# Kernel tuning notes

Measured on AMD Instinct MI355X. Metric: run time of the kernel, lower is better.

Reference implementation:

```python
import jax, jax.numpy as jnp
import numpy as np

S, B, D, H, DH, E, F = 2048, 2, 512, 8, 64, 8, 1024
TOPK = 2


def setup_inputs() -> dict:
    key = jax.random.key(0)
    ks = jax.random.split(key, 12)
    rn = lambda k, shp, s=0.02: jax.random.normal(k, shp, jnp.float32) * s
    # RoPE tables (half-split convention): (S, DH)
    pos = jnp.arange(S, dtype=jnp.float32)[:, None]
    inv_freq = 1.0 / (10000.0 ** (jnp.arange(0, DH, 2, dtype=jnp.float32) / DH))
    ang = pos * inv_freq[None, :]                       # (S, DH//2)
    cos = jnp.concatenate([jnp.cos(ang), jnp.cos(ang)], axis=-1)
    sin = jnp.concatenate([jnp.sin(ang), jnp.sin(ang)], axis=-1)
    return {
        "src": jax.random.normal(ks[0], (S, B, D), jnp.float32),
        "cos": cos, "sin": sin,
        "Wq": rn(ks[1], (D, D)), "bq": jnp.zeros((D,), jnp.float32),
        "Wk": rn(ks[2], (D, D)), "bk": jnp.zeros((D,), jnp.float32),
        "Wv": rn(ks[3], (D, D)), "bv": jnp.zeros((D,), jnp.float32),
        "Wo": rn(ks[4], (D, D)), "bo": jnp.zeros((D,), jnp.float32),
        "ln1_g": jnp.ones((D,), jnp.float32), "ln1_b": jnp.zeros((D,), jnp.float32),
        "ln2_g": jnp.ones((D,), jnp.float32), "ln2_b": jnp.zeros((D,), jnp.float32),
        "Wg": rn(ks[5], (D, E)),
        "W1": rn(ks[6], (E, D, F)), "B1": jnp.zeros((E, F), jnp.float32),
        "W2": rn(ks[7], (E, F, D)), "B2": jnp.zeros((E, D), jnp.float32),
    }


def _layernorm(x, g, b, eps=1e-5):
    m = x.mean(-1, keepdims=True)
    v = ((x - m) ** 2).mean(-1, keepdims=True)
    return (x - m) * jax.lax.rsqrt(v + eps) * g + b


def _rotate_half(x):
    x1, x2 = jnp.split(x, 2, axis=-1)
    return jnp.concatenate([-x2, x1], axis=-1)


def _forward(src, cos, sin, Wq, bq, Wk, bk, Wv, bv, Wo, bo,
             ln1_g, ln1_b, ln2_g, ln2_b, Wg, W1, B1, W2, B2):
    # ---- RoPE self-attention ----
    q = (src @ Wq + bq).reshape(S, B, H, DH)
    k = (src @ Wk + bk).reshape(S, B, H, DH)
    v = (src @ Wv + bv).reshape(S, B, H, DH)
    c = cos[:, None, None, :]
    s = sin[:, None, None, :]
    q = q * c + _rotate_half(q) * s
    k = k * c + _rotate_half(k) * s
    scores = jnp.einsum("sbhd,tbhd->bhst", q, k) / jnp.sqrt(jnp.float32(DH))
    attn = jax.nn.softmax(scores, axis=-1)              # (B,H,S,S)
    ctx = jnp.einsum("bhst,tbhd->sbhd", attn, v).reshape(S, B, D)
    attn_out = ctx @ Wo + bo
    x = _layernorm(src + attn_out, ln1_g, ln1_b)
    # ---- MoE feed-forward (top-k softmax gating) ----
    xt = x.reshape(S * B, D)                            # (N, D)
    probs = jax.nn.softmax(xt @ Wg, axis=-1)            # (N, E)
    top_v, top_i = jax.lax.top_k(probs, TOPK)           # (N, TOPK)
    top_v = top_v / top_v.sum(-1, keepdims=True)
    N = S * B
    gates = jnp.zeros((N, E), jnp.float32).at[
        jnp.arange(N)[:, None], top_i].add(top_v)       # (N, E)
    h = jax.nn.relu(jnp.einsum("nd,edf->nef", xt, W1) + B1[None])   # (N,E,F)
    eo = jnp.einsum("nef,efd->ned", h, W2) + B2[None]               # (N,E,D)
    moe_out = jnp.einsum("ne,ned->nd", gates, eo).reshape(S, B, D)
    return _layernorm(x + moe_out, ln2_g, ln2_b)


def reference(src, cos, sin, Wq, bq, Wk, bk, Wv, bv, Wo, bo,
              ln1_g, ln1_b, ln2_g, ln2_b, Wg, W1, B1, W2, B2):
    return _forward(src, cos, sin, Wq, bq, Wk, bk, Wv, bv, Wo, bo,
                    ln1_g, ln1_b, ln2_g, ln2_b, Wg, W1, B1, W2, B2)
```

## Files before the change

kernel.cpp:

```cpp
#include <hip/hip_runtime.h>
#include <math.h>

#define S_  2048
#define B_  2
#define D_  512
#define H_  8
#define DH_ 64
#define E_  8
#define F_  1024
#define N_  4096
#define NPAIR_ 8192

typedef __attribute__((ext_vector_type(4))) float f32x4;
typedef __attribute__((ext_vector_type(8))) short short8;
typedef unsigned short u16;

__device__ __forceinline__ u16 f2bf(float f) {
  unsigned u = __builtin_bit_cast(unsigned, f);
  u += 0x7fffu + ((u >> 16) & 1u);
  return (u16)(u >> 16);
}
__device__ __forceinline__ float bf2f(u16 h) {
  unsigned u = ((unsigned)h) << 16;
  return __builtin_bit_cast(float, u);
}

__global__ __launch_bounds__(256) void src_split(const float* __restrict__ in,
                                                 u16* __restrict__ hi,
                                                 u16* __restrict__ lo) {
  size_t i = ((size_t)blockIdx.x * 256 + threadIdx.x) * 8;
  float f[8];
  *(float4*)&f[0] = *(const float4*)&in[i];
  *(float4*)&f[4] = *(const float4*)&in[i + 4];
  short8 h, l;
#pragma unroll
  for (int j = 0; j < 8; ++j) {
    u16 a = f2bf(f[j]);
    h[j] = (short)a;
    l[j] = (short)f2bf(f[j] - bf2f(a));
  }
  *(short8*)&hi[i] = h;
  *(short8*)&lo[i] = l;
}

__global__ __launch_bounds__(256) void wsplit_t(const float* __restrict__ W,
                                                u16* __restrict__ Whi,
                                                u16* __restrict__ Wlo,
                                                int Nn, int K) {
  __shared__ u16 Th[64][72];
  __shared__ u16 Tl[64][72];
  int kb = blockIdx.y * 64, nb = blockIdx.x * 64;
  int r = threadIdx.x >> 2, c0 = (threadIdx.x & 3) * 16;
  const float* wp = &W[(size_t)(kb + r) * Nn + nb + c0];
#pragma unroll
  for (int c = 0; c < 16; c += 4) {
    float4 t = *(const float4*)&wp[c];
    float f[4] = {t.x, t.y, t.z, t.w};
#pragma unroll
    for (int j = 0; j < 4; ++j) {
      u16 a = f2bf(f[j]);
      Th[r][c0 + c + j] = a;
      Tl[r][c0 + c + j] = f2bf(f[j] - bf2f(a));
    }
  }
  __syncthreads();
  short8 h0, h1, l0, l1;
#pragma unroll
  for (int j = 0; j < 8; ++j) {
    h0[j] = (short)Th[c0 + j][r];     h1[j] = (short)Th[c0 + 8 + j][r];
    l0[j] = (short)Tl[c0 + j][r];     l1[j] = (short)Tl[c0 + 8 + j][r];
  }
  size_t ob = (size_t)(nb + r) * K + kb + c0;
  *(short8*)&Whi[ob] = h0;  *(short8*)&Whi[ob + 8] = h1;
  *(short8*)&Wlo[ob] = l0;  *(short8*)&Wlo[ob + 8] = l1;
}

__global__ __launch_bounds__(256) void wtrans(const float* __restrict__ W,
                                              u16* __restrict__ Wt,
                                              int K, int Nn) {
  size_t eo = (size_t)blockIdx.z * K * Nn;
  __shared__ u16 T[64][72];
  int kb = blockIdx.y * 64, nb = blockIdx.x * 64;
  int r = threadIdx.x >> 2, c0 = (threadIdx.x & 3) * 16;
  const float* wp = &W[eo + (size_t)(kb + r) * Nn + nb + c0];
#pragma unroll
  for (int c = 0; c < 16; c += 4) {
    float4 t = *(const float4*)&wp[c];
    T[r][c0 + c + 0] = f2bf(t.x);
    T[r][c0 + c + 1] = f2bf(t.y);
    T[r][c0 + c + 2] = f2bf(t.z);
    T[r][c0 + c + 3] = f2bf(t.w);
  }
  __syncthreads();
  short8 s0, s1;
#pragma unroll
  for (int j = 0; j < 8; ++j) {
    s0[j] = (short)T[c0 + j][r];
    s1[j] = (short)T[c0 + 8 + j][r];
  }
  *(short8*)&Wt[eo + (size_t)(nb + r) * K + kb + c0] = s0;
  *(short8*)&Wt[eo + (size_t)(nb + r) * K + kb + c0 + 8] = s1;
}

__global__ __launch_bounds__(256) void qkv_mfma(const u16* __restrict__ Ah_g,
                                                const u16* __restrict__ Al_g,
                                                const u16* __restrict__ Bh_g,
                                                const u16* __restrict__ Bl_g,
                                                const float* __restrict__ bq,
                                                const float* __restrict__ bk,
                                                const float* __restrict__ bv,
                                                const float* __restrict__ cosb,
                                                const float* __restrict__ sinb,
                                                u16* __restrict__ qh, u16* __restrict__ ql,
                                                u16* __restrict__ kh, u16* __restrict__ kl,
                                                u16* __restrict__ vb) {
  __shared__ u16 Ah[128][40], Al[128][40], Bh[128][40], Bl[128][40];
  int tid = threadIdx.x;
  int w = tid >> 6, l = tid & 63;
  int wr = w >> 1, wc = w & 1;
  int lg = l >> 4, lx = l & 15;
  int m0 = blockIdx.x * 128, n0 = blockIdx.y * 128;
  int sr = tid >> 1, s16 = (tid & 1) * 16;
  const u16* Aph = Ah_g + (size_t)(m0 + sr) * 512;
  const u16* Apl = Al_g + (size_t)(m0 + sr) * 512;
  const u16* Bph = Bh_g + (size_t)(n0 + sr) * 512;
  const u16* Bpl = Bl_g + (size_t)(n0 + sr) * 512;
  f32x4 acc[4][4];
#pragma unroll
  for (int m = 0; m < 4; ++m)
#pragma unroll
    for (int n = 0; n < 4; ++n) acc[m][n] = (f32x4){0.f, 0.f, 0.f, 0.f};
  short8 ah0 = *(const short8*)&Aph[s16];
  short8 ah1 = *(const short8*)&Aph[s16 + 8];
  short8 al0 = *(const short8*)&Apl[s16];
  short8 al1 = *(const short8*)&Apl[s16 + 8];
  short8 bh0 = *(const short8*)&Bph[s16];
  short8 bh1 = *(const short8*)&Bph[s16 + 8];
  short8 bl0 = *(const short8*)&Bpl[s16];
  short8 bl1 = *(const short8*)&Bpl[s16 + 8];
  for (int k0 = 0; k0 < 512; k0 += 32) {
    __syncthreads();
    *(short8*)&Ah[sr][s16] = ah0; *(short8*)&Ah[sr][s16 + 8] = ah1;
    *(short8*)&Al[sr][s16] = al0; *(short8*)&Al[sr][s16 + 8] = al1;
    *(short8*)&Bh[sr][s16] = bh0; *(short8*)&Bh[sr][s16 + 8] = bh1;
    *(short8*)&Bl[sr][s16] = bl0; *(short8*)&Bl[sr][s16 + 8] = bl1;
    __syncthreads();
    if (k0 + 32 < 512) {
      int ko = k0 + 32 + s16;
      ah0 = *(const short8*)&Aph[ko]; ah1 = *(const short8*)&Aph[ko + 8];
      al0 = *(const short8*)&Apl[ko]; al1 = *(const short8*)&Apl[ko + 8];
      bh0 = *(const short8*)&Bph[ko]; bh1 = *(const short8*)&Bph[ko + 8];
      bl0 = *(const short8*)&Bpl[ko]; bl1 = *(const short8*)&Bpl[ko + 8];
    }
    short8 fah[4], fal[4], fbh[4], fbl[4];
#pragma unroll
    for (int m = 0; m < 4; ++m) {
      fah[m] = *(const short8*)&Ah[wr * 64 + m * 16 + lx][lg * 8];
      fal[m] = *(const short8*)&Al[wr * 64 + m * 16 + lx][lg * 8];
    }
#pragma unroll
    for (int n = 0; n < 4; ++n) {
      fbh[n] = *(const short8*)&Bh[wc * 64 + n * 16 + lx][lg * 8];
      fbl[n] = *(const short8*)&Bl[wc * 64 + n * 16 + lx][lg * 8];
    }
#pragma unroll
    for (int m = 0; m < 4; ++m)
#pragma unroll
      for (int n = 0; n < 4; ++n) {
        acc[m][n] = __builtin_amdgcn_mfma_f32_16x16x32_bf16(fah[m], fbh[n], acc[m][n], 0, 0, 0);
        acc[m][n] = __builtin_amdgcn_mfma_f32_16x16x32_bf16(fal[m], fbh[n], acc[m][n], 0, 0, 0);
        acc[m][n] = __builtin_amdgcn_mfma_f32_16x16x32_bf16(fah[m], fbl[n], acc[m][n], 0, 0, 0);
      }
  }
  int tcolbase = n0 + wc * 64;
  int tsel = tcolbase >> 9;
  int hbase = tcolbase & 511;
  const float* bias = (tsel == 0) ? bq : (tsel == 1) ? bk : bv;
  if (tsel == 2) {
#pragma unroll
    for (int m = 0; m < 4; ++m)
#pragma unroll
      for (int i = 0; i < 4; ++i) {
        int row = m0 + wr * 64 + m * 16 + lg * 4 + i;
#pragma unroll
        for (int n = 0; n < 4; ++n) {
          int col = hbase + n * 16 + lx;
          vb[(size_t)row * 512 + col] = f2bf(acc[m][n][i] + bias[col]);
        }
      }
  } else {
    u16* oh = tsel ? kh : qh;
    u16* ol = tsel ? kl : ql;
    float qsc = tsel ? 1.f : 0.125f;
#pragma unroll
    for (int m = 0; m < 4; ++m)
#pragma unroll
      for (int i = 0; i < 4; ++i) {
        int row = m0 + wr * 64 + m * 16 + lg * 4 + i;
        int s = row >> 1;
#pragma unroll
        for (int n = 0; n < 2; ++n) {
          int dln = n * 16 + lx;
          float c  = cosb[s * 64 + dln];
          float sn = sinb[s * 64 + dln];
          float a  = acc[m][n][i]     + bias[hbase + dln];
          float b2 = acc[m][n + 2][i] + bias[hbase + dln + 32];
          float ra = (a * c - b2 * sn) * qsc;
          float rb = (b2 * c + a * sn) * qsc;
          size_t ix = (size_t)row * 512 + hbase + dln;
          u16 rah = f2bf(ra);
          oh[ix] = rah; ol[ix] = f2bf(ra - bf2f(rah));
          u16 rbh = f2bf(rb);
          oh[ix + 32] = rbh; ol[ix + 32] = f2bf(rb - bf2f(rbh));
        }
      }
  }
}

__global__ __launch_bounds__(512) void attn_mfma2(const u16* __restrict__ qh,
                                                  const u16* __restrict__ ql,
                                                  const u16* __restrict__ kh,
                                                  const u16* __restrict__ kl,
                                                  const u16* __restrict__ vbuf,
                                                  u16* __restrict__ poh,
                                                  u16* __restrict__ pol,
                                                  float* __restrict__ pml) {
  __shared__ u16 Khi[64][72];
  __shared__ u16 Klo[64][72];
  __shared__ u16 Vt[64][72];
  __shared__ unsigned P2[8][16][32];
  int tid = threadIdx.x;
  int w = tid >> 6, l = tid & 63;
  int lg = l >> 4, lx = l & 15;
  int f = blockIdx.x;
  int xcd = f & 7, j = f >> 3;
  int slab = xcd + 8 * (j & 3);
  int qt = j >> 2;
  int bh = slab >> 1, kvh = slab & 1;
  int b = bh >> 3, h = bh & 7;

  short8 qfh[2], qfl[2];
  {
    int qrow = qt * 128 + w * 16 + lx;
    size_t qo = (size_t)(qrow * 2 + b) * 512 + h * 64 + lg * 8;
    qfh[0] = *(const short8*)&qh[qo];
    qfh[1] = *(const short8*)&qh[qo + 32];
    qfl[0] = *(const short8*)&ql[qo];
    qfl[1] = *(const short8*)&ql[qo + 32];
  }

  f32x4 o_acc[4];
#pragma unroll
  for (int dg = 0; dg < 4; ++dg) o_acc[dg] = (f32x4){0.f, 0.f, 0.f, 0.f};
  float m_run = -1e30f, l_run = 0.f;

  int kvr = tid >> 3, ds4 = (tid & 7) * 8;
  int kvc = tid & 63, dsg = (tid >> 6) * 8;
  int psw = (lx & 7) << 2;

  short8 rkh, rkl, rv;
  {
    int t0 = kvh * 1024;
    size_t ko = (size_t)((t0 + kvr) * 2 + b) * 512 + h * 64 + ds4;
    rkh = *(const short8*)&kh[ko];
    rkl = *(const short8*)&kl[ko];
    size_t vo = (size_t)((t0 + kvc) * 2 + b) * 512 + h * 64 + dsg;
    rv = *(const short8*)&vbuf[vo];
  }

  for (int tt = 0; tt < 1024; tt += 64) {
    __syncthreads();
    *(short8*)&Khi[kvr][ds4] = rkh;
    *(short8*)&Klo[kvr][ds4] = rkl;
#pragma unroll
    for (int c = 0; c < 8; ++c) Vt[dsg + c][kvc] = (u16)rv[c];
    __syncthreads();
    if (tt + 64 < 1024) {
      int t0 = kvh * 1024 + tt + 64;
      size_t ko = (size_t)((t0 + kvr) * 2 + b) * 512 + h * 64 + ds4;
      rkh = *(const short8*)&kh[ko];
      rkl = *(const short8*)&kl[ko];
      size_t vo = (size_t)((t0 + kvc) * 2 + b) * 512 + h * 64 + dsg;
      rv = *(const short8*)&vbuf[vo];
    }

    f32x4 sc[4];
#pragma unroll
    for (int cg = 0; cg < 4; ++cg) {
      short8 kf0 = *(const short8*)&Khi[cg * 16 + lx][lg * 8];
      short8 kf1 = *(const short8*)&Khi[cg * 16 + lx][32 + lg * 8];
      short8 kg0 = *(const short8*)&Klo[cg * 16 + lx][lg * 8];
      short8 kg1 = *(const short8*)&Klo[cg * 16 + lx][32 + lg * 8];
      f32x4 a = (f32x4){0.f, 0.f, 0.f, 0.f};
      a = __builtin_amdgcn_mfma_f32_16x16x32_bf16(kf0, qfh[0], a, 0, 0, 0);
      a = __builtin_amdgcn_mfma_f32_16x16x32_bf16(kf1, qfh[1], a, 0, 0, 0);
      a = __builtin_amdgcn_mfma_f32_16x16x32_bf16(kf0, qfl[0], a, 0, 0, 0);
      a = __builtin_amdgcn_mfma_f32_16x16x32_bf16(kf1, qfl[1], a, 0, 0, 0);
      a = __builtin_amdgcn_mfma_f32_16x16x32_bf16(kg0, qfh[0], a, 0, 0, 0);
      a = __builtin_amdgcn_mfma_f32_16x16x32_bf16(kg1, qfh[1], a, 0, 0, 0);
      sc[cg] = a;
    }

    float tm = sc[0][0];
#pragma unroll
    for (int cg = 0; cg < 4; ++cg)
#pragma unroll
      for (int i = 0; i < 4; ++i) tm = fmaxf(tm, sc[cg][i]);
    tm = fmaxf(tm, __shfl_xor(tm, 16));
    tm = fmaxf(tm, __shfl_xor(tm, 32));
    float mn = fmaxf(m_run, tm);
    float corr = __expf(m_run - mn);
    m_run = mn;
    float ts = 0.f;
#pragma unroll
    for (int cg = 0; cg < 4; ++cg)
#pragma unroll
      for (int i = 0; i < 4; ++i) {
        float pv = __expf(sc[cg][i] - mn);
        sc[cg][i] = pv;
        ts += pv;
      }
    ts += __shfl_xor(ts, 16);
    ts += __shfl_xor(ts, 32);
    l_run = l_run * corr + ts;
#pragma unroll
    for (int dg = 0; dg < 4; ++dg) o_acc[dg] *= corr;

#pragma unroll
    for (int cg = 0; cg < 4; ++cg)
#pragma unroll
      for (int t = 0; t < 2; ++t) {
        unsigned dw = (unsigned)f2bf(sc[cg][2 * t]) |
                      ((unsigned)f2bf(sc[cg][2 * t + 1]) << 16);
        P2[w][lx][(8 * cg + 2 * lg + t) ^ psw] = dw;
      }
    short8 pf0 = *(const short8*)&P2[w][lx][(4 * lg) ^ psw];
    short8 pf1 = *(const short8*)&P2[w][lx][(16 + 4 * lg) ^ psw];

#pragma unroll
    for (int dg = 0; dg < 4; ++dg) {
      short8 v0 = *(const short8*)&Vt[dg * 16 + lx][lg * 8];
      short8 v1 = *(const short8*)&Vt[dg * 16 + lx][32 + lg * 8];
      o_acc[dg] = __builtin_amdgcn_mfma_f32_16x16x32_bf16(v0, pf0, o_acc[dg], 0, 0, 0);
      o_acc[dg] = __builtin_amdgcn_mfma_f32_16x16x32_bf16(v1, pf1, o_acc[dg], 0, 0, 0);
    }
  }

  {
    int qrow = qt * 128 + w * 16 + lx;
    int row2 = qrow * 2 + b;
    size_t base = (size_t)kvh * ((size_t)N_ * D_) + (size_t)row2 * 512 + h * 64;
#pragma unroll
    for (int dg = 0; dg < 4; ++dg)
#pragma unroll
      for (int i = 0; i < 4; ++i) {
        int d = dg * 16 + 4 * lg + i;
        float val = o_acc[dg][i];
        u16 hi = f2bf(val);
        poh[base + d] = hi;
        pol[base + d] = f2bf(val - bf2f(hi));
      }
    if (lg == 0) {
      int u = row2 * 8 + h;
      pml[(size_t)kvh * 65536 + u * 2 + 0] = m_run;
      pml[(size_t)kvh * 65536 + u * 2 + 1] = l_run;
    }
  }
}

__global__ __launch_bounds__(256) void merge_attn2(const u16* __restrict__ poh,
                                                   const u16* __restrict__ pol,
                                                   const float* __restrict__ pml,
                                                   u16* __restrict__ ch,
                                                   u16* __restrict__ cl) {
  int u = blockIdx.x * 4 + (threadIdx.x >> 6);
  int lane = threadIdx.x & 63;
  float m0 = pml[u * 2], l0 = pml[u * 2 + 1];
  float m1 = pml[65536 + u * 2], l1 = pml[65536 + u * 2 + 1];
  float m = fmaxf(m0, m1);
  float e0 = __expf(m0 - m), e1 = __expf(m1 - m);
  float inv = 1.f / (l0 * e0 + l1 * e1);
  int n = u >> 3, h = u & 7;
  size_t base = (size_t)n * 512 + h * 64 + lane;
  const size_t PO1 = (size_t)N_ * D_;
  float v0 = bf2f(poh[base]) + bf2f(pol[base]);
  float v1 = bf2f(poh[PO1 + base]) + bf2f(pol[PO1 + base]);
  float val = (v0 * e0 + v1 * e1) * inv;
  u16 hi = f2bf(val);
  ch[base] = hi;
  cl[base] = f2bf(val - bf2f(hi));
}

__global__ __launch_bounds__(256) void wo_mfma(const u16* __restrict__ Ah_g,
                                               const u16* __restrict__ Al_g,
                                               const u16* __restrict__ Bh_g,
                                               const u16* __restrict__ Bl_g,
                                               const float* __restrict__ bias,
                                               float* __restrict__ C) {
  __shared__ u16 Ah[128][40], Al[128][40], Bh[128][40], Bl[128][40];
  int tid = threadIdx.x;
  int w = tid >> 6, l = tid & 63;
  int wr = w >> 1, wc = w & 1;
  int lg = l >> 4, lx = l & 15;
  int m0 = blockIdx.x * 128, n0 = blockIdx.y * 128;
  int sr = tid >> 1, s16 = (tid & 1) * 16;
  const u16* Aph = Ah_g + (size_t)(m0 + sr) * 512;
  const u16* Apl = Al_g + (size_t)(m0 + sr) * 512;
  const u16* Bph = Bh_g + (size_t)(n0 + sr) * 512;
  const u16* Bpl = Bl_g + (size_t)(n0 + sr) * 512;
  f32x4 acc[4][4];
#pragma unroll
  for (int m = 0; m < 4; ++m)
#pragma unroll
    for (int n = 0; n < 4; ++n) acc[m][n] = (f32x4){0.f, 0.f, 0.f, 0.f};
  short8 ah0 = *(const short8*)&Aph[s16];
  short8 ah1 = *(const short8*)&Aph[s16 + 8];
  short8 al0 = *(const short8*)&Apl[s16];
  short8 al1 = *(const short8*)&Apl[s16 + 8];
  short8 bh0 = *(const short8*)&Bph[s16];
  short8 bh1 = *(const short8*)&Bph[s16 + 8];
  short8 bl0 = *(const short8*)&Bpl[s16];
  short8 bl1 = *(const short8*)&Bpl[s16 + 8];
  for (int k0 = 0; k0 < 512; k0 += 32) {
    __syncthreads();
    *(short8*)&Ah[sr][s16] = ah0; *(short8*)&Ah[sr][s16 + 8] = ah1;
    *(short8*)&Al[sr][s16] = al0; *(short8*)&Al[sr][s16 + 8] = al1;
    *(short8*)&Bh[sr][s16] = bh0; *(short8*)&Bh[sr][s16 + 8] = bh1;
    *(short8*)&Bl[sr][s16] = bl0; *(short8*)&Bl[sr][s16 + 8] = bl1;
    __syncthreads();
    if (k0 + 32 < 512) {
      int ko = k0 + 32 + s16;
      ah0 = *(const short8*)&Aph[ko]; ah1 = *(const short8*)&Aph[ko + 8];
      al0 = *(const short8*)&Apl[ko]; al1 = *(const short8*)&Apl[ko + 8];
      bh0 = *(const short8*)&Bph[ko]; bh1 = *(const short8*)&Bph[ko + 8];
      bl0 = *(const short8*)&Bpl[ko]; bl1 = *(const short8*)&Bpl[ko + 8];
    }
    short8 fah[4], fal[4], fbh[4], fbl[4];
#pragma unroll
    for (int m = 0; m < 4; ++m) {
      fah[m] = *(const short8*)&Ah[wr * 64 + m * 16 + lx][lg * 8];
      fal[m] = *(const short8*)&Al[wr * 64 + m * 16 + lx][lg * 8];
    }
#pragma unroll
    for (int n = 0; n < 4; ++n) {
      fbh[n] = *(const short8*)&Bh[wc * 64 + n * 16 + lx][lg * 8];
      fbl[n] = *(const short8*)&Bl[wc * 64 + n * 16 + lx][lg * 8];
    }
#pragma unroll
    for (int m = 0; m < 4; ++m)
#pragma unroll
      for (int n = 0; n < 4; ++n) {
        acc[m][n] = __builtin_amdgcn_mfma_f32_16x16x32_bf16(fah[m], fbh[n], acc[m][n], 0, 0, 0);
        acc[m][n] = __builtin_amdgcn_mfma_f32_16x16x32_bf16(fal[m], fbh[n], acc[m][n], 0, 0, 0);
        acc[m][n] = __builtin_amdgcn_mfma_f32_16x16x32_bf16(fah[m], fbl[n], acc[m][n], 0, 0, 0);
      }
  }
#pragma unroll
  for (int m = 0; m < 4; ++m)
#pragma unroll
    for (int i = 0; i < 4; ++i) {
      int row = m0 + wr * 64 + m * 16 + lg * 4 + i;
#pragma unroll
      for (int n = 0; n < 4; ++n) {
        int col = n0 + wc * 64 + n * 16 + lx;
        C[(size_t)row * 512 + col] = acc[m][n][i] + bias[col];
      }
    }
}

__global__ __launch_bounds__(256) void ln_res_gate(const float* __restrict__ a,
                                                   const float* __restrict__ b,
                                                   const float* __restrict__ g,
                                                   const float* __restrict__ beta,
                                                   const float* __restrict__ Wg,
                                                   float* __restrict__ out,
                                                   u16* __restrict__ obf,
                                                   float* __restrict__ gp,
                                                   int* __restrict__ tope) {
  int n = blockIdx.x * 4 + (threadIdx.x >> 6);
  int lane = threadIdx.x & 63;
  float v[8];
  float s = 0.f;
#pragma unroll
  for (int i = 0; i < 8; ++i) {
    int d = lane + 64 * i;
    v[i] = a[(size_t)n * D_ + d] + b[(size_t)n * D_ + d];
    s += v[i];
  }
#pragma unroll
  for (int m = 32; m; m >>= 1) s += __shfl_xor(s, m);
  float mean = s * (1.f / D_);
  float s2 = 0.f;
#pragma unroll
  for (int i = 0; i < 8; ++i) { float t = v[i] - mean; s2 += t * t; }
#pragma unroll
  for (int m = 32; m; m >>= 1) s2 += __shfl_xor(s2, m);
  float r = rsqrtf(s2 * (1.f / D_) + 1e-5f);
  float p[E_] = {};
#pragma unroll
  for (int i = 0; i < 8; ++i) {
    int d = lane + 64 * i;
    float val = (v[i] - mean) * r * g[d] + beta[d];
    out[(size_t)n * D_ + d] = val;
    obf[(size_t)n * D_ + d] = f2bf(val);
    const float* wr = &Wg[(size_t)d * E_];
#pragma unroll
    for (int e = 0; e < E_; ++e) p[e] += val * wr[e];
  }
#pragma unroll
  for (int e = 0; e < E_; ++e)
#pragma unroll
    for (int m = 32; m; m >>= 1) p[e] += __shfl_xor(p[e], m);
  if (lane == 0) {
    float mx = p[0];
#pragma unroll
    for (int e = 1; e < E_; ++e) mx = fmaxf(mx, p[e]);
    float q[E_];
#pragma unroll
    for (int e = 0; e < E_; ++e) q[e] = expf(p[e] - mx);
    int e1 = 0;
#pragma unroll
    for (int e = 1; e < E_; ++e) if (q[e] > q[e1]) e1 = e;
    int e2 = (e1 == 0) ? 1 : 0;
#pragma unroll
    for (int e = 0; e < E_; ++e) if (e != e1 && q[e] > q[e2]) e2 = e;
    float denom = q[e1] + q[e2];
    gp[n * 2] = q[e1] / denom;
    gp[n * 2 + 1] = q[e2] / denom;
    tope[n] = e1 | (e2 << 8);
  }
}

__global__ __launch_bounds__(256) void ln2_final(const float* __restrict__ x,
                                                 const u16* __restrict__ mp,
                                                 const float* __restrict__ g,
                                                 const float* __restrict__ beta,
                                                 float* __restrict__ out) {
  int n = blockIdx.x * 4 + (threadIdx.x >> 6);
  int lane = threadIdx.x & 63;
  float v[8];
  float s = 0.f;
#pragma unroll
  for (int i = 0; i < 8; ++i) {
    int d = lane + 64 * i;
    v[i] = x[(size_t)n * D_ + d] + bf2f(mp[(size_t)(2 * n) * D_ + d]) +
           bf2f(mp[(size_t)(2 * n + 1) * D_ + d]);
    s += v[i];
  }
#pragma unroll
  for (int m = 32; m; m >>= 1) s += __shfl_xor(s, m);
  float mean = s * (1.f / D_);
  float s2 = 0.f;
#pragma unroll
  for (int i = 0; i < 8; ++i) { float t = v[i] - mean; s2 += t * t; }
#pragma unroll
  for (int m = 32; m; m >>= 1) s2 += __shfl_xor(s2, m);
  float r = rsqrtf(s2 * (1.f / D_) + 1e-5f);
#pragma unroll
  for (int i = 0; i < 8; ++i) {
    int d = lane + 64 * i;
    out[(size_t)n * D_ + d] = (v[i] - mean) * r * g[d] + beta[d];
  }
}

__global__ __launch_bounds__(256) void route_build(const int* __restrict__ tope,
                                                   int* __restrict__ cnt,
                                                   int* __restrict__ lst) {
  int e = blockIdx.x;
  __shared__ int wsum[4];
  __shared__ int basem;
  int tid = threadIdx.x;
  int w = tid >> 6, lane = tid & 63;
  if (tid == 0) basem = 0;
  __syncthreads();
  for (int c0 = 0; c0 < N_; c0 += 256) {
    int n = c0 + tid;
    int te = tope[n];
    int e1 = te & 0xff, e2 = (te >> 8) & 0xff;
    bool m2 = (e2 == e);
    bool flag = (e1 == e) || m2;
    unsigned long long mask = __ballot(flag);
    int wpre = __popcll(mask & ((1ull << lane) - 1ull));
    if (lane == 0) wsum[w] = __popcll(mask);
    __syncthreads();
    int woff = 0;
    for (int i = 0; i < w; ++i) woff += wsum[i];
    int total = wsum[0] + wsum[1] + wsum[2] + wsum[3];
    if (flag) lst[e * N_ + basem + woff + wpre] = n * 2 + (m2 ? 1 : 0);
    __syncthreads();
    if (tid == 0) basem += total;
    __syncthreads();
  }
  if (tid == 0) cnt[e] = basem;
}

template <int MODE>
__global__ __launch_bounds__(256) void moe_mfma(const u16* __restrict__ Abase,
                                                const u16* __restrict__ Wt,
                                                const float* __restrict__ bias,
                                                const float* __restrict__ gp,
                                                u16* __restrict__ outp,
                                                const int* __restrict__ cnt,
                                                const int* __restrict__ lst) {
  constexpr int K  = MODE ? 1024 : 512;
  constexpr int Nn = MODE ? 512 : 1024;
  constexpr int NT = Nn / 128;
  constexpr int NI = K / 32;
  int fidx = blockIdx.x;
  int e = fidx & 7;
  int r = fidx >> 3;
  int nt = r % NT;
  int mt = r / NT;
  int c = cnt[e];
  int m0 = mt * 64;
  if (m0 >= c) return;
  int off = 0;
#pragma unroll
  for (int i = 0; i < E_; ++i) if (i < e) off += cnt[i];
  int n0 = nt * 128;
  __shared__ u16 As[64][40];
  __shared__ u16 Bs[128][40];
  int tid = threadIdx.x;
  int w = tid >> 6, l = tid & 63;
  int lg = l >> 4, lx = l & 15;
  int arow = tid >> 2, aseg = (tid & 3) * 8;
  int brow = tid >> 1, bseg = (tid & 1) * 16;
  int ar = m0 + arow; if (ar >= c) ar = c - 1;
  const u16* Ap;
  if (MODE == 0) Ap = Abase + (size_t)(lst[e * N_ + ar] >> 1) * 512 + aseg;
  else           Ap = Abase + (size_t)(off + ar) * 1024 + aseg;
  const u16* Bp = Wt + (size_t)e * K * Nn + (size_t)(n0 + brow) * K + bseg;

  f32x4 acc[4][2];
#pragma unroll
  for (int m = 0; m < 4; ++m)
#pragma unroll
    for (int n = 0; n < 2; ++n) acc[m][n] = (f32x4){0.f, 0.f, 0.f, 0.f};

  short8 pa  = *(const short8*)&Ap[0];
  short8 pb0 = *(const short8*)&Bp[0];
  short8 pb1 = *(const short8*)&Bp[8];
  for (int kk = 0; kk < NI; ++kk) {
    __syncthreads();
    *(short8*)&As[arow][aseg] = pa;
    *(short8*)&Bs[brow][bseg] = pb0;
    *(short8*)&Bs[brow][bseg + 8] = pb1;
    __syncthreads();
    if (kk + 1 < NI) {
      int ko = (kk + 1) * 32;
      pa  = *(const short8*)&Ap[ko];
      pb0 = *(const short8*)&Bp[ko];
      pb1 = *(const short8*)&Bp[ko + 8];
    }
    short8 af[4], bf[2];
#pragma unroll
    for (int m = 0; m < 4; ++m)
      af[m] = *(const short8*)&As[m * 16 + lx][lg * 8];
#pragma unroll
    for (int n = 0; n < 2; ++n)
      bf[n] = *(const short8*)&Bs[w * 32 + n * 16 + lx][lg * 8];
#pragma unroll
    for (int m = 0; m < 4; ++m)
#pragma unroll
      for (int n = 0; n < 2; ++n)
        acc[m][n] = __builtin_amdgcn_mfma_f32_16x16x32_bf16(af[m], bf[n], acc[m][n], 0, 0, 0);
  }
#pragma unroll
  for (int m = 0; m < 4; ++m)
#pragma unroll
    for (int i = 0; i < 4; ++i) {
      int rr = m0 + m * 16 + lg * 4 + i;
      if (rr < c) {
#pragma unroll
        for (int n = 0; n < 2; ++n) {
          int col = n0 + w * 32 + n * 16 + lx;
          float val = acc[m][n][i] + bias[e * Nn + col];
          if (MODE == 0) {
            outp[(size_t)(off + rr) * 1024 + col] = f2bf(fmaxf(val, 0.f));
          } else {
            int p = lst[e * N_ + rr];
            outp[(size_t)p * 512 + col] = f2bf(gp[p] * val);
          }
        }
      }
    }
}

extern "C" void kernel_launch(void* const* d_in, const int* in_sizes, int n_in,
                              void* d_out, int out_size, void* d_ws, size_t ws_size,
                              hipStream_t stream) {
  const float* src  = (const float*)d_in[0];
  const float* cosb = (const float*)d_in[1];
  const float* sinb = (const float*)d_in[2];
  const float* Wq   = (const float*)d_in[3];
  const float* bq   = (const float*)d_in[4];
  const float* Wk   = (const float*)d_in[5];
  const float* bk   = (const float*)d_in[6];
  const float* Wv   = (const float*)d_in[7];
  const float* bv   = (const float*)d_in[8];
  const float* Wo   = (const float*)d_in[9];
  const float* bo   = (const float*)d_in[10];
  const float* ln1g = (const float*)d_in[11];
  const float* ln1b = (const float*)d_in[12];
  const float* ln2g = (const float*)d_in[13];
  const float* ln2b = (const float*)d_in[14];
  const float* Wg   = (const float*)d_in[15];
  const float* W1   = (const float*)d_in[16];
  const float* B1   = (const float*)d_in[17];
  const float* W2   = (const float*)d_in[18];
  const float* B2   = (const float*)d_in[19];
  float* out = (float*)d_out;
  char* wsb = (char*)d_ws;

  const size_t MB1 = 1u << 20;
  u16* sh   = (u16*)(wsb + 0 * MB1);
  u16* sl   = (u16*)(wsb + 4 * MB1);
  u16* qhb  = (u16*)(wsb + 8 * MB1);
  u16* qlb  = (u16*)(wsb + 12 * MB1);
  u16* khb  = (u16*)(wsb + 16 * MB1);
  u16* klb  = (u16*)(wsb + 20 * MB1);
  u16* vbuf = (u16*)(wsb + 24 * MB1);
  u16* poh  = (u16*)(wsb + 28 * MB1);
  u16* pol  = (u16*)(wsb + 36 * MB1);
  float* pml = (float*)(wsb + 44 * MB1);
  float* aob = (float*)(wsb + 28 * MB1);
  float* xb  = (float*)(wsb + 36 * MB1);
  u16* xbf   = (u16*)(wsb + 44 * MB1);
  u16* Wqkv_hi = (u16*)(wsb + 48 * MB1);
  u16* Wqkv_lo = (u16*)(wsb + 48 * MB1 + 1572864);
  u16* Wo_hi   = (u16*)(wsb + 48 * MB1 + 3145728);
  u16* Wo_lo   = (u16*)(wsb + 48 * MB1 + 3670016);
  u16* W1t     = (u16*)(wsb + 52 * MB1);
  u16* W2t     = (u16*)(wsb + 28 * MB1);
  float* gpb   = (float*)(wsb + 60 * MB1);
  int* cnt     = (int*)(wsb + 60 * MB1 + 32768);
  int* lst     = (int*)(wsb + 60 * MB1 + 32768 + 64);
  int* tope    = (int*)(wsb + 60 * MB1 + 32768 + 64 + 131072);
  u16* ch  = sh;
  u16* cl  = sl;
  u16* hbf = (u16*)(wsb + 8 * MB1);
  u16* mp  = (u16*)(wsb + 0 * MB1);

  dim3 blk(256);
  src_split<<<dim3(1024), blk, 0, stream>>>(src, sh, sl);
  wsplit_t<<<dim3(8, 8), blk, 0, stream>>>(Wq, Wqkv_hi, Wqkv_lo, 512, 512);
  wsplit_t<<<dim3(8, 8), blk, 0, stream>>>(Wk, Wqkv_hi + 512 * 512, Wqkv_lo + 512 * 512, 512, 512);
  wsplit_t<<<dim3(8, 8), blk, 0, stream>>>(Wv, Wqkv_hi + 1024 * 512, Wqkv_lo + 1024 * 512, 512, 512);
  wsplit_t<<<dim3(8, 8), blk, 0, stream>>>(Wo, Wo_hi, Wo_lo, 512, 512);
  qkv_mfma<<<dim3(32, 12), blk, 0, stream>>>(sh, sl, Wqkv_hi, Wqkv_lo, bq, bk, bv,
                                             cosb, sinb, qhb, qlb, khb, klb, vbuf);
  attn_mfma2<<<dim3(512), dim3(512), 0, stream>>>(qhb, qlb, khb, klb, vbuf, poh, pol, pml);
  merge_attn2<<<dim3(8192), blk, 0, stream>>>(poh, pol, pml, ch, cl);
  wo_mfma<<<dim3(32, 4), blk, 0, stream>>>(ch, cl, Wo_hi, Wo_lo, bo, aob);
  ln_res_gate<<<dim3(1024), blk, 0, stream>>>(src, aob, ln1g, ln1b, Wg, xb, xbf, gpb, tope);
  wtrans<<<dim3(8, 16, 8), blk, 0, stream>>>(W2, W2t, 1024, 512);
  wtrans<<<dim3(16, 8, 8), blk, 0, stream>>>(W1, W1t, 512, 1024);
  route_build<<<dim3(8), blk, 0, stream>>>(tope, cnt, lst);
  moe_mfma<0><<<dim3(8 * 8 * 64), blk, 0, stream>>>(xbf, W1t, B1, gpb, hbf, cnt, lst);
  moe_mfma<1><<<dim3(8 * 4 * 64), blk, 0, stream>>>(hbf, W2t, B2, gpb, mp, cnt, lst);
  ln2_final<<<dim3(1024), blk, 0, stream>>>(xb, mp, ln2g, ln2b, out);
}
```

Before: 227.2 us.

## Double-buffer attention K/V tiles and XCD-swizzle GEMM block mapping

The attention kernel now keeps two LDS buffers for K/V tiles, so the next tile is written to shared memory while the current one is consumed. This drops one of the two barriers per iteration. The QKV and Wo GEMMs switch to a 1D grid whose mapping puts four consecutive M-tiles on each XCD, aiming to improve L2 reuse of A rows. LDS use in the attention kernel roughly doubles for K/V, which may lower occupancy.

```diff
diff --git a/kernel.cpp b/kernel.cpp
--- a/kernel.cpp
+++ b/kernel.cpp
@@ -119,7 +119,11 @@
   int w = tid >> 6, l = tid & 63;
   int wr = w >> 1, wc = w & 1;
   int lg = l >> 4, lx = l & 15;
-  int m0 = blockIdx.x * 128, n0 = blockIdx.y * 128;
+  int f = blockIdx.x;
+  int xcd = f & 7, rr = f >> 3;
+  int mt = xcd * 4 + (rr & 3);
+  int nt = rr >> 2;
+  int m0 = mt * 128, n0 = nt * 128;
   int sr = tid >> 1, s16 = (tid & 1) * 16;
   const u16* Aph = Ah_g + (size_t)(m0 + sr) * 512;
   const u16* Apl = Al_g + (size_t)(m0 + sr) * 512;
@@ -225,9 +229,9 @@
                                                   u16* __restrict__ poh,
                                                   u16* __restrict__ pol,
                                                   float* __restrict__ pml) {
-  __shared__ u16 Khi[64][72];
-  __shared__ u16 Klo[64][72];
-  __shared__ u16 Vt[64][72];
+  __shared__ u16 Khi[2][64][72];
+  __shared__ u16 Klo[2][64][72];
+  __shared__ u16 Vt[2][64][72];
   __shared__ unsigned P2[8][16][32];
   int tid = threadIdx.x;
   int w = tid >> 6, l = tid & 63;
@@ -266,31 +270,43 @@
     rkl = *(const short8*)&kl[ko];
     size_t vo = (size_t)((t0 + kvc) * 2 + b) * 512 + h * 64 + dsg;
     rv = *(const short8*)&vbuf[vo];
-  }
-
-  for (int tt = 0; tt < 1024; tt += 64) {
-    __syncthreads();
-    *(short8*)&Khi[kvr][ds4] = rkh;
-    *(short8*)&Klo[kvr][ds4] = rkl;
-#pragma unroll
-    for (int c = 0; c < 8; ++c) Vt[dsg + c][kvc] = (u16)rv[c];
-    __syncthreads();
-    if (tt + 64 < 1024) {
-      int t0 = kvh * 1024 + tt + 64;
-      size_t ko = (size_t)((t0 + kvr) * 2 + b) * 512 + h * 64 + ds4;
-      rkh = *(const short8*)&kh[ko];
-      rkl = *(const short8*)&kl[ko];
-      size_t vo = (size_t)((t0 + kvc) * 2 + b) * 512 + h * 64 + dsg;
-      rv = *(const short8*)&vbuf[vo];
+    *(short8*)&Khi[0][kvr][ds4] = rkh;
+    *(short8*)&Klo[0][kvr][ds4] = rkl;
+#pragma unroll
+    for (int c = 0; c < 8; ++c) Vt[0][dsg + c][kvc] = (u16)rv[c];
+    t0 += 64;
+    ko = (size_t)((t0 + kvr) * 2 + b) * 512 + h * 64 + ds4;
+    rkh = *(const short8*)&kh[ko];
+    rkl = *(const short8*)&kl[ko];
+    vo = (size_t)((t0 + kvc) * 2 + b) * 512 + h * 64 + dsg;
+    rv = *(const short8*)&vbuf[vo];
+  }
+
+  for (int it = 0; it < 16; ++it) {
+    int cur = it & 1;
+    __syncthreads();
+    if (it + 1 < 16) {
+      *(short8*)&Khi[cur ^ 1][kvr][ds4] = rkh;
+      *(short8*)&Klo[cur ^ 1][kvr][ds4] = rkl;
+#pragma unroll
+      for (int c = 0; c < 8; ++c) Vt[cur ^ 1][dsg + c][kvc] = (u16)rv[c];
+      if (it + 2 < 16) {
+        int t0 = kvh * 1024 + (it + 2) * 64;
+        size_t ko = (size_t)((t0 + kvr) * 2 + b) * 512 + h * 64 + ds4;
+        rkh = *(const short8*)&kh[ko];
+        rkl = *(const short8*)&kl[ko];
+        size_t vo = (size_t)((t0 + kvc) * 2 + b) * 512 + h * 64 + dsg;
+        rv = *(const short8*)&vbuf[vo];
+      }
     }
 
     f32x4 sc[4];
 #pragma unroll
     for (int cg = 0; cg < 4; ++cg) {
-      short8 kf0 = *(const short8*)&Khi[cg * 16 + lx][lg * 8];
-      short8 kf1 = *(const short8*)&Khi[cg * 16 + lx][32 + lg * 8];
-      short8 kg0 = *(const short8*)&Klo[cg * 16 + lx][lg * 8];
-      short8 kg1 = *(const short8*)&Klo[cg * 16 + lx][32 + lg * 8];
+      short8 kf0 = *(const short8*)&Khi[cur][cg * 16 + lx][lg * 8];
+      short8 kf1 = *(const short8*)&Khi[cur][cg * 16 + lx][32 + lg * 8];
+      short8 kg0 = *(const short8*)&Klo[cur][cg * 16 + lx][lg * 8];
+      short8 kg1 = *(const short8*)&Klo[cur][cg * 16 + lx][32 + lg * 8];
       f32x4 a = (f32x4){0.f, 0.f, 0.f, 0.f};
       a = __builtin_amdgcn_mfma_f32_16x16x32_bf16(kf0, qfh[0], a, 0, 0, 0);
       a = __builtin_amdgcn_mfma_f32_16x16x32_bf16(kf1, qfh[1], a, 0, 0, 0);
@@ -339,8 +355,8 @@
 
 #pragma unroll
     for (int dg = 0; dg < 4; ++dg) {
-      short8 v0 = *(const short8*)&Vt[dg * 16 + lx][lg * 8];
-      short8 v1 = *(const short8*)&Vt[dg * 16 + lx][32 + lg * 8];
+      short8 v0 = *(const short8*)&Vt[cur][dg * 16 + lx][lg * 8];
+      short8 v1 = *(const short8*)&Vt[cur][dg * 16 + lx][32 + lg * 8];
       o_acc[dg] = __builtin_amdgcn_mfma_f32_16x16x32_bf16(v0, pf0, o_acc[dg], 0, 0, 0);
       o_acc[dg] = __builtin_amdgcn_mfma_f32_16x16x32_bf16(v1, pf1, o_acc[dg], 0, 0, 0);
     }
@@ -402,7 +418,10 @@
   int w = tid >> 6, l = tid & 63;
   int wr = w >> 1, wc = w & 1;
   int lg = l >> 4, lx = l & 15;
-  int m0 = blockIdx.x * 128, n0 = blockIdx.y * 128;
+  int f = blockIdx.x;
+  int xcd = f & 7, rr = f >> 3;
+  int m0 = (xcd * 4 + (rr & 3)) * 128;
+  int n0 = (rr >> 2) * 128;
   int sr = tid >> 1, s16 = (tid & 1) * 16;
   const u16* Aph = Ah_g + (size_t)(m0 + sr) * 512;
   const u16* Apl = Al_g + (size_t)(m0 + sr) * 512;
@@ -747,11 +766,11 @@
   wsplit_t<<<dim3(8, 8), blk, 0, stream>>>(Wk, Wqkv_hi + 512 * 512, Wqkv_lo + 512 * 512, 512, 512);
   wsplit_t<<<dim3(8, 8), blk, 0, stream>>>(Wv, Wqkv_hi + 1024 * 512, Wqkv_lo + 1024 * 512, 512, 512);
   wsplit_t<<<dim3(8, 8), blk, 0, stream>>>(Wo, Wo_hi, Wo_lo, 512, 512);
-  qkv_mfma<<<dim3(32, 12), blk, 0, stream>>>(sh, sl, Wqkv_hi, Wqkv_lo, bq, bk, bv,
-                                             cosb, sinb, qhb, qlb, khb, klb, vbuf);
+  qkv_mfma<<<dim3(384), blk, 0, stream>>>(sh, sl, Wqkv_hi, Wqkv_lo, bq, bk, bv,
+                                          cosb, sinb, qhb, qlb, khb, klb, vbuf);
   attn_mfma2<<<dim3(512), dim3(512), 0, stream>>>(qhb, qlb, khb, klb, vbuf, poh, pol, pml);
   merge_attn2<<<dim3(8192), blk, 0, stream>>>(poh, pol, pml, ch, cl);
-  wo_mfma<<<dim3(32, 4), blk, 0, stream>>>(ch, cl, Wo_hi, Wo_lo, bo, aob);
+  wo_mfma<<<dim3(128), blk, 0, stream>>>(ch, cl, Wo_hi, Wo_lo, bo, aob);
   ln_res_gate<<<dim3(1024), blk, 0, stream>>>(src, aob, ln1g, ln1b, Wg, xb, xbf, gpb, tope);
   wtrans<<<dim3(8, 16, 8), blk, 0, stream>>>(W2, W2t, 1024, 512);
   wtrans<<<dim3(16, 8, 8), blk, 0, stream>>>(W1, W1t, 512, 1024);
```

New measurement: 226.9 us. About the same (-0.1%).

## Split attention KV into four chunks and remap GEMM blocks per XCD

Applied to the files above, without the earlier changes.

Attention now splits the key/value sequence into four 512-token chunks instead of two, doubling the grid to 1024 blocks, and the merge kernel combines four partial results. The qkv and wo GEMMs use a 1D grid remapped so each XCD handles a contiguous group of M tiles, which should improve L2 reuse. The MFMA sections get s_setprio hints, P stores are widened to 64-bit with a new swizzle, and the workspace layout is reshuffled to hold the larger partial buffers. Trade-offs are more partial-output traffic and a heavier merge pass in exchange for better occupancy in attention.

```diff
diff --git a/kernel.cpp b/kernel.cpp
--- a/kernel.cpp
+++ b/kernel.cpp
@@ -119,7 +119,11 @@
   int w = tid >> 6, l = tid & 63;
   int wr = w >> 1, wc = w & 1;
   int lg = l >> 4, lx = l & 15;
-  int m0 = blockIdx.x * 128, n0 = blockIdx.y * 128;
+  int f = blockIdx.x;
+  int xcd = f & 7, rr = f >> 3;
+  int mt = xcd * 4 + (rr & 3);
+  int nt = rr >> 2;
+  int m0 = mt * 128, n0 = nt * 128;
   int sr = tid >> 1, s16 = (tid & 1) * 16;
   const u16* Aph = Ah_g + (size_t)(m0 + sr) * 512;
   const u16* Apl = Al_g + (size_t)(m0 + sr) * 512;
@@ -234,9 +238,9 @@
   int lg = l >> 4, lx = l & 15;
   int f = blockIdx.x;
   int xcd = f & 7, j = f >> 3;
-  int slab = xcd + 8 * (j & 3);
-  int qt = j >> 2;
-  int bh = slab >> 1, kvh = slab & 1;
+  int slab = xcd + 8 * (j & 7);
+  int qt = j >> 3;
+  int bh = slab >> 2, kvh = slab & 3;
   int b = bh >> 3, h = bh & 7;
 
   short8 qfh[2], qfl[2];
@@ -256,11 +260,11 @@
 
   int kvr = tid >> 3, ds4 = (tid & 7) * 8;
   int kvc = tid & 63, dsg = (tid >> 6) * 8;
-  int psw = (lx & 7) << 2;
+  int psw = (lx & 3) << 3;
 
   short8 rkh, rkl, rv;
   {
-    int t0 = kvh * 1024;
+    int t0 = kvh * 512;
     size_t ko = (size_t)((t0 + kvr) * 2 + b) * 512 + h * 64 + ds4;
     rkh = *(const short8*)&kh[ko];
     rkl = *(const short8*)&kl[ko];
@@ -268,15 +272,15 @@
     rv = *(const short8*)&vbuf[vo];
   }
 
-  for (int tt = 0; tt < 1024; tt += 64) {
+  for (int tt = 0; tt < 512; tt += 64) {
     __syncthreads();
     *(short8*)&Khi[kvr][ds4] = rkh;
     *(short8*)&Klo[kvr][ds4] = rkl;
 #pragma unroll
     for (int c = 0; c < 8; ++c) Vt[dsg + c][kvc] = (u16)rv[c];
     __syncthreads();
-    if (tt + 64 < 1024) {
-      int t0 = kvh * 1024 + tt + 64;
+    if (tt + 64 < 512) {
+      int t0 = kvh * 512 + tt + 64;
       size_t ko = (size_t)((t0 + kvr) * 2 + b) * 512 + h * 64 + ds4;
       rkh = *(const short8*)&kh[ko];
       rkl = *(const short8*)&kl[ko];
@@ -285,6 +289,7 @@
     }
 
     f32x4 sc[4];
+    __builtin_amdgcn_s_setprio(1);
 #pragma unroll
     for (int cg = 0; cg < 4; ++cg) {
       short8 kf0 = *(const short8*)&Khi[cg * 16 + lx][lg * 8];
@@ -300,6 +305,7 @@
       a = __builtin_amdgcn_mfma_f32_16x16x32_bf16(kg1, qfh[1], a, 0, 0, 0);
       sc[cg] = a;
     }
+    __builtin_amdgcn_s_setprio(0);
 
     float tm = sc[0][0];
 #pragma unroll
@@ -327,16 +333,16 @@
     for (int dg = 0; dg < 4; ++dg) o_acc[dg] *= corr;
 
 #pragma unroll
-    for (int cg = 0; cg < 4; ++cg)
-#pragma unroll
-      for (int t = 0; t < 2; ++t) {
-        unsigned dw = (unsigned)f2bf(sc[cg][2 * t]) |
-                      ((unsigned)f2bf(sc[cg][2 * t + 1]) << 16);
-        P2[w][lx][(8 * cg + 2 * lg + t) ^ psw] = dw;
-      }
+    for (int cg = 0; cg < 4; ++cg) {
+      unsigned d0 = (unsigned)f2bf(sc[cg][0]) | ((unsigned)f2bf(sc[cg][1]) << 16);
+      unsigned d1 = (unsigned)f2bf(sc[cg][2]) | ((unsigned)f2bf(sc[cg][3]) << 16);
+      uint2 dd; dd.x = d0; dd.y = d1;
+      *(uint2*)&P2[w][lx][(8 * cg + 2 * lg) ^ psw] = dd;
+    }
     short8 pf0 = *(const short8*)&P2[w][lx][(4 * lg) ^ psw];
     short8 pf1 = *(const short8*)&P2[w][lx][(16 + 4 * lg) ^ psw];
 
+    __builtin_amdgcn_s_setprio(1);
 #pragma unroll
     for (int dg = 0; dg < 4; ++dg) {
       short8 v0 = *(const short8*)&Vt[dg * 16 + lx][lg * 8];
@@ -344,6 +350,7 @@
       o_acc[dg] = __builtin_amdgcn_mfma_f32_16x16x32_bf16(v0, pf0, o_acc[dg], 0, 0, 0);
       o_acc[dg] = __builtin_amdgcn_mfma_f32_16x16x32_bf16(v1, pf1, o_acc[dg], 0, 0, 0);
     }
+    __builtin_amdgcn_s_setprio(0);
   }
 
   {
@@ -368,24 +375,34 @@
   }
 }
 
-__global__ __launch_bounds__(256) void merge_attn2(const u16* __restrict__ poh,
+__global__ __launch_bounds__(256) void merge_attn4(const u16* __restrict__ poh,
                                                    const u16* __restrict__ pol,
                                                    const float* __restrict__ pml,
                                                    u16* __restrict__ ch,
                                                    u16* __restrict__ cl) {
   int u = blockIdx.x * 4 + (threadIdx.x >> 6);
   int lane = threadIdx.x & 63;
-  float m0 = pml[u * 2], l0 = pml[u * 2 + 1];
-  float m1 = pml[65536 + u * 2], l1 = pml[65536 + u * 2 + 1];
-  float m = fmaxf(m0, m1);
-  float e0 = __expf(m0 - m), e1 = __expf(m1 - m);
-  float inv = 1.f / (l0 * e0 + l1 * e1);
+  float mv[4], lv[4];
+#pragma unroll
+  for (int k = 0; k < 4; ++k) {
+    mv[k] = pml[(size_t)k * 65536 + u * 2 + 0];
+    lv[k] = pml[(size_t)k * 65536 + u * 2 + 1];
+  }
+  float m = fmaxf(fmaxf(mv[0], mv[1]), fmaxf(mv[2], mv[3]));
+  float e[4], den = 0.f;
+#pragma unroll
+  for (int k = 0; k < 4; ++k) { e[k] = __expf(mv[k] - m); den += lv[k] * e[k]; }
+  float inv = 1.f / den;
   int n = u >> 3, h = u & 7;
   size_t base = (size_t)n * 512 + h * 64 + lane;
   const size_t PO1 = (size_t)N_ * D_;
-  float v0 = bf2f(poh[base]) + bf2f(pol[base]);
-  float v1 = bf2f(poh[PO1 + base]) + bf2f(pol[PO1 + base]);
-  float val = (v0 * e0 + v1 * e1) * inv;
+  float val = 0.f;
+#pragma unroll
+  for (int k = 0; k < 4; ++k) {
+    float v = bf2f(poh[(size_t)k * PO1 + base]) + bf2f(pol[(size_t)k * PO1 + base]);
+    val += v * e[k];
+  }
+  val *= inv;
   u16 hi = f2bf(val);
   ch[base] = hi;
   cl[base] = f2bf(val - bf2f(hi));
@@ -402,7 +419,10 @@
   int w = tid >> 6, l = tid & 63;
   int wr = w >> 1, wc = w & 1;
   int lg = l >> 4, lx = l & 15;
-  int m0 = blockIdx.x * 128, n0 = blockIdx.y * 128;
+  int f = blockIdx.x;
+  int xcd = f & 7, rr = f >> 3;
+  int m0 = (xcd * 4 + (rr & 3)) * 128;
+  int n0 = (rr >> 2) * 128;
   int sr = tid >> 1, s16 = (tid & 1) * 16;
   const u16* Aph = Ah_g + (size_t)(m0 + sr) * 512;
   const u16* Apl = Al_g + (size_t)(m0 + sr) * 512;
@@ -713,45 +733,45 @@
   char* wsb = (char*)d_ws;
 
   const size_t MB1 = 1u << 20;
-  u16* sh   = (u16*)(wsb + 0 * MB1);
-  u16* sl   = (u16*)(wsb + 4 * MB1);
-  u16* qhb  = (u16*)(wsb + 8 * MB1);
-  u16* qlb  = (u16*)(wsb + 12 * MB1);
-  u16* khb  = (u16*)(wsb + 16 * MB1);
-  u16* klb  = (u16*)(wsb + 20 * MB1);
-  u16* vbuf = (u16*)(wsb + 24 * MB1);
-  u16* poh  = (u16*)(wsb + 28 * MB1);
+  u16* qhb  = (u16*)(wsb + 0 * MB1);
+  u16* qlb  = (u16*)(wsb + 4 * MB1);
+  u16* khb  = (u16*)(wsb + 8 * MB1);
+  u16* klb  = (u16*)(wsb + 12 * MB1);
+  u16* vbuf = (u16*)(wsb + 16 * MB1);
+  u16* Wqkv_hi = (u16*)(wsb + 20 * MB1);
+  u16* Wqkv_lo = (u16*)(wsb + 20 * MB1 + 1572864);
+  u16* poh  = (u16*)(wsb + 20 * MB1);
   u16* pol  = (u16*)(wsb + 36 * MB1);
-  float* pml = (float*)(wsb + 44 * MB1);
-  float* aob = (float*)(wsb + 28 * MB1);
-  float* xb  = (float*)(wsb + 36 * MB1);
-  u16* xbf   = (u16*)(wsb + 44 * MB1);
-  u16* Wqkv_hi = (u16*)(wsb + 48 * MB1);
-  u16* Wqkv_lo = (u16*)(wsb + 48 * MB1 + 1572864);
-  u16* Wo_hi   = (u16*)(wsb + 48 * MB1 + 3145728);
-  u16* Wo_lo   = (u16*)(wsb + 48 * MB1 + 3670016);
-  u16* W1t     = (u16*)(wsb + 52 * MB1);
-  u16* W2t     = (u16*)(wsb + 28 * MB1);
-  float* gpb   = (float*)(wsb + 60 * MB1);
-  int* cnt     = (int*)(wsb + 60 * MB1 + 32768);
-  int* lst     = (int*)(wsb + 60 * MB1 + 32768 + 64);
-  int* tope    = (int*)(wsb + 60 * MB1 + 32768 + 64 + 131072);
-  u16* ch  = sh;
-  u16* cl  = sl;
-  u16* hbf = (u16*)(wsb + 8 * MB1);
-  u16* mp  = (u16*)(wsb + 0 * MB1);
+  u16* ch   = (u16*)(wsb + 0 * MB1);
+  u16* cl   = (u16*)(wsb + 4 * MB1);
+  float* aob = (float*)(wsb + 16 * MB1);
+  float* xb  = (float*)(wsb + 24 * MB1);
+  u16* xbf   = (u16*)(wsb + 32 * MB1);
+  u16* W1t   = (u16*)(wsb + 36 * MB1);
+  u16* W2t   = (u16*)(wsb + 44 * MB1);
+  u16* sh    = (u16*)(wsb + 52 * MB1);
+  u16* sl    = (u16*)(wsb + 56 * MB1);
+  u16* Wo_hi = (u16*)(wsb + 52 * MB1);
+  u16* Wo_lo = (u16*)(wsb + 52 * MB1 + 524288);
+  float* pml = (float*)(wsb + 53 * MB1);
+  float* gpb = (float*)(wsb + 54 * MB1);
+  int* cnt   = (int*)(wsb + 54 * MB1 + 32768);
+  int* lst   = (int*)(wsb + 54 * MB1 + 32768 + 64);
+  int* tope  = (int*)(wsb + 54 * MB1 + 32768 + 64 + 131072);
+  u16* hbf = (u16*)(wsb + 0 * MB1);
+  u16* mp  = (u16*)(wsb + 32 * MB1);
 
   dim3 blk(256);
   src_split<<<dim3(1024), blk, 0, stream>>>(src, sh, sl);
   wsplit_t<<<dim3(8, 8), blk, 0, stream>>>(Wq, Wqkv_hi, Wqkv_lo, 512, 512);
   wsplit_t<<<dim3(8, 8), blk, 0, stream>>>(Wk, Wqkv_hi + 512 * 512, Wqkv_lo + 512 * 512, 512, 512);
   wsplit_t<<<dim3(8, 8), blk, 0, stream>>>(Wv, Wqkv_hi + 1024 * 512, Wqkv_lo + 1024 * 512, 512, 512);
+  qkv_mfma<<<dim3(384), blk, 0, stream>>>(sh, sl, Wqkv_hi, Wqkv_lo, bq, bk, bv,
+                                          cosb, sinb, qhb, qlb, khb, klb, vbuf);
   wsplit_t<<<dim3(8, 8), blk, 0, stream>>>(Wo, Wo_hi, Wo_lo, 512, 512);
-  qkv_mfma<<<dim3(32, 12), blk, 0, stream>>>(sh, sl, Wqkv_hi, Wqkv_lo, bq, bk, bv,
-                                             cosb, sinb, qhb, qlb, khb, klb, vbuf);
-  attn_mfma2<<<dim3(512), dim3(512), 0, stream>>>(qhb, qlb, khb, klb, vbuf, poh, pol, pml);
-  merge_attn2<<<dim3(8192), blk, 0, stream>>>(poh, pol, pml, ch, cl);
-  wo_mfma<<<dim3(32, 4), blk, 0, stream>>>(ch, cl, Wo_hi, Wo_lo, bo, aob);
+  attn_mfma2<<<dim3(1024), dim3(512), 0, stream>>>(qhb, qlb, khb, klb, vbuf, poh, pol, pml);
+  merge_attn4<<<dim3(8192), blk, 0, stream>>>(poh, pol, pml, ch, cl);
+  wo_mfma<<<dim3(128), blk, 0, stream>>>(ch, cl, Wo_hi, Wo_lo, bo, aob);
   ln_res_gate<<<dim3(1024), blk, 0, stream>>>(src, aob, ln1g, ln1b, Wg, xb, xbf, gpb, tope);
   wtrans<<<dim3(8, 16, 8), blk, 0, stream>>>(W2, W2t, 1024, 512);
   wtrans<<<dim3(16, 8, 8), blk, 0, stream>>>(W1, W1t, 512, 1024);
```

After: 245.9 us. +8.2%, slower.
